# Kernel tuning notes

Measured on AMD Instinct MI355X. Metric: run time of the kernel, lower is better.

## Reference

```python
import jax, jax.numpy as jnp
import numpy as np

N_NODES = 50000
N_EDGES = 600000
N_GRAPHS = 1000


def setup_inputs() -> dict:
    key = jax.random.key(0)
    ks = jax.random.split(key, 16)
    x = jax.random.normal(ks[0], (N_NODES, 37), dtype=jnp.float32)
    edge_index = jax.random.randint(ks[1], (2, N_EDGES), 0, N_NODES, dtype=jnp.int64)
    batch = jnp.sort(jax.random.randint(ks[2], (N_NODES,), 0, N_GRAPHS, dtype=jnp.int64))

    def lin(k, fi, fo):
        s = 1.0 / np.sqrt(fi)
        kw, kb = jax.random.split(k)
        W = jax.random.uniform(kw, (fi, fo), minval=-s, maxval=s, dtype=jnp.float32)
        b = jax.random.uniform(kb, (fo,), minval=-s, maxval=s, dtype=jnp.float32)
        return W, b

    W1, b1 = lin(ks[3], 37, 64)
    W2, b2 = lin(ks[4], 64, 128)
    W3, b3 = lin(ks[5], 128, 64)
    Wf1, bf1 = lin(ks[6], 64, 128)
    Wf2, bf2 = lin(ks[7], 128, 64)
    gamma = jnp.ones((64,), jnp.float32)
    beta = jnp.zeros((64,), jnp.float32)
    return dict(x=x, edge_index=edge_index, batch=batch,
                W1=W1, b1=b1, W2=W2, b2=b2, W3=W3, b3=b3,
                Wf1=Wf1, bf1=bf1, Wf2=Wf2, bf2=bf2, gamma=gamma, beta=beta)


def _gcn_conv(x, W, b, rows, cols, norm, n_nodes):
    # PyG GCNConv: out_i = sum_j norm_ij * (x_j W) + b, over A + I edges
    h = x @ W
    msg = h[rows] * norm[:, None]          # [E+N, F_out] gather
    out = jax.ops.segment_sum(msg, cols, num_segments=n_nodes)  # scatter-add
    return out + b


def reference(x, edge_index, batch,
              W1, b1, W2, b2, W3, b3,
              Wf1, bf1, Wf2, bf2, gamma, beta):
    n = x.shape[0]
    loop = jnp.arange(n, dtype=edge_index.dtype)
    rows = jnp.concatenate([edge_index[0], loop])  # source nodes (+ self loops)
    cols = jnp.concatenate([edge_index[1], loop])  # target nodes
    deg = jax.ops.segment_sum(jnp.ones_like(cols, dtype=x.dtype), cols, num_segments=n)
    dinv = jnp.where(deg > 0, jax.lax.rsqrt(jnp.maximum(deg, 1e-12)), 0.0)
    norm = dinv[rows] * dinv[cols]

    h = jax.nn.relu(_gcn_conv(x, W1, b1, rows, cols, norm, n))
    h = jax.nn.relu(_gcn_conv(h, W2, b2, rows, cols, norm, n))
    h = jax.nn.relu(_gcn_conv(h, W3, b3, rows, cols, norm, n))

    # global mean pool per graph
    sums = jax.ops.segment_sum(h, batch, num_segments=N_GRAPHS)
    cnts = jax.ops.segment_sum(jnp.ones((n,), h.dtype), batch, num_segments=N_GRAPHS)
    g = sums / jnp.maximum(cnts, 1.0)[:, None]

    g = jax.nn.relu(g @ Wf1 + bf1)
    g = jax.nn.relu(g @ Wf2 + bf2)

    mu = jnp.mean(g, axis=-1, keepdims=True)
    var = jnp.mean(jnp.square(g - mu), axis=-1, keepdims=True)
    return (g - mu) * jax.lax.rsqrt(var + 1e-5) * gamma + beta
```

## Files before the change

### kernel.cpp

```cpp
#include <hip/hip_runtime.h>
#include <hip/hip_bf16.h>



__global__ __launch_bounds__(256)
void hist_kernel(const int* __restrict__ cols, int* __restrict__ counts, int E,
                 const int* __restrict__ batch, int* __restrict__ gcnt, int n) {
    int idx = blockIdx.x * 256 + threadIdx.x;
    if (idx < E) {
        atomicAdd(&counts[cols[idx]], 1);
    } else {
        int i = idx - E;
        if (i < n) atomicAdd(&gcnt[batch[i]], 1);
    }
}


__global__ __launch_bounds__(1024)
void scan1_kernel(const int* __restrict__ counts, int* __restrict__ offs,
                  int* __restrict__ bsum, int n) {
    __shared__ int tmp[1024];
    int i = blockIdx.x * 1024 + threadIdx.x;
    int v = (i < n) ? counts[i] : 0;
    tmp[threadIdx.x] = v;
    __syncthreads();
    for (int o = 1; o < 1024; o <<= 1) {
        int x = (threadIdx.x >= o) ? tmp[threadIdx.x - o] : 0;
        __syncthreads();
        tmp[threadIdx.x] += x;
        __syncthreads();
    }
    if (i < n) offs[i] = tmp[threadIdx.x] - v;
    if (threadIdx.x == 1023) bsum[blockIdx.x] = tmp[1023];
}

__global__ __launch_bounds__(1024)
void scan_meta_kernel(int* __restrict__ bsum, int nb,
                      const int* __restrict__ gcnt, int* __restrict__ goff,
                      int ng, int n_nodes) {
    __shared__ int ta[1024];
    __shared__ int tb[1024];
    int t = threadIdx.x;
    int va = (t < nb) ? bsum[t] : 0;
    int vb = (t < ng) ? gcnt[t] : 0;
    ta[t] = va;
    tb[t] = vb;
    __syncthreads();
    for (int o = 1; o < 1024; o <<= 1) {
        int xa = (t >= o) ? ta[t - o] : 0;
        int xb = (t >= o) ? tb[t - o] : 0;
        __syncthreads();
        ta[t] += xa;
        tb[t] += xb;
        __syncthreads();
    }
    if (t < nb) bsum[t] = ta[t] - va;
    if (t < ng) goff[t] = tb[t] - vb;
    if (t == 0) goff[ng] = n_nodes;
}

__global__ __launch_bounds__(256)
void scan3_kernel(int* __restrict__ offs, const int* __restrict__ bsum,
                  const int* __restrict__ counts, float* __restrict__ dinv,
                  int n, int E) {
    int i = blockIdx.x * 256 + threadIdx.x;
    if (i < n) {
        offs[i] += bsum[i >> 10];
        dinv[i] = rsqrtf((float)(counts[i] + 1));
    }
    if (i == 0) offs[n] = E;
}

__global__ __launch_bounds__(256)
void fill_kernel(const int* __restrict__ rows, const int* __restrict__ cols,
                 const int* __restrict__ offs, int* __restrict__ cursor,
                 int* __restrict__ esrc, int E) {
    int e = blockIdx.x * 256 + threadIdx.x;
    if (e >= E) return;
    int r = rows[e], c = cols[e];
    int pos = offs[c] + atomicAdd(&cursor[c], 1);
    esrc[pos] = r;
}


template <int F, int WSRC>
__global__ __launch_bounds__(256)
void agg_kernel(const float* __restrict__ g, const int* __restrict__ offs,
                const int* __restrict__ esrc, const float* __restrict__ dinv,
                const float* __restrict__ bias, int do_relu,
                float* __restrict__ out, int n) {
    static_assert(F <= 64, "one lane per feature");
    int wid  = threadIdx.x >> 6;
    int lane = threadIdx.x & 63;
    int node = blockIdx.x * 4 + wid;
    if (node >= n) return;
    int c = (lane < F) ? lane : (F - 1);
    float dv = dinv[node];
    float a0 = (WSRC ? dv : 1.0f) * g[(size_t)node * F + c];
    float a1 = 0.f, a2 = 0.f, a3 = 0.f, a4 = 0.f, a5 = 0.f, a6 = 0.f, a7 = 0.f;
    int s = offs[node], e = offs[node + 1];
    int k = s;
    for (; k + 7 < e; k += 8) {
        int s0 = esrc[k],     s1 = esrc[k + 1], s2 = esrc[k + 2], s3 = esrc[k + 3];
        int s4 = esrc[k + 4], s5 = esrc[k + 5], s6 = esrc[k + 6], s7 = esrc[k + 7];
        float w0 = WSRC ? dinv[s0] : 1.f, w1 = WSRC ? dinv[s1] : 1.f;
        float w2 = WSRC ? dinv[s2] : 1.f, w3 = WSRC ? dinv[s3] : 1.f;
        float w4 = WSRC ? dinv[s4] : 1.f, w5 = WSRC ? dinv[s5] : 1.f;
        float w6 = WSRC ? dinv[s6] : 1.f, w7 = WSRC ? dinv[s7] : 1.f;
        a0 += w0 * g[(size_t)s0 * F + c];
        a1 += w1 * g[(size_t)s1 * F + c];
        a2 += w2 * g[(size_t)s2 * F + c];
        a3 += w3 * g[(size_t)s3 * F + c];
        a4 += w4 * g[(size_t)s4 * F + c];
        a5 += w5 * g[(size_t)s5 * F + c];
        a6 += w6 * g[(size_t)s6 * F + c];
        a7 += w7 * g[(size_t)s7 * F + c];
    }
    for (; k < e; ++k) {
        int s0 = esrc[k];
        float w0 = WSRC ? dinv[s0] : 1.f;
        a0 += w0 * g[(size_t)s0 * F + c];
    }
    float v = (((a0 + a1) + (a2 + a3)) + ((a4 + a5) + (a6 + a7))) * dv;
    if (bias)    v += bias[c];
    if (do_relu) v = fmaxf(v, 0.f);
    if (lane < F) out[(size_t)node * F + c] = v;
}


template <int K, int F>
__global__ __launch_bounds__(256)
void mm_kernel(const float* __restrict__ X, const float* __restrict__ W,
               const float* __restrict__ bias, const float* __restrict__ dscale,
               int do_relu, float* __restrict__ out, int n) {
    constexpr int ROWS = 32;
    constexpr int CG = F / 4;
    __shared__ __align__(16) float Ws[K * F];
    __shared__ __align__(16) float xs[ROWS * K];
    int r0 = blockIdx.x * ROWS;
    for (int i = threadIdx.x; i < K * F; i += 256) Ws[i] = W[i];
    int nrow = n - r0; if (nrow > ROWS) nrow = ROWS;
    const float* Xb = X + (size_t)r0 * K;
    int tot = nrow * K;
    for (int i = threadIdx.x; i < tot; i += 256) xs[i] = Xb[i];
    __syncthreads();
    for (int idx = threadIdx.x; idx < ROWS * CG; idx += 256) {
        int r = idx / CG, cg = idx % CG;
        if (r >= nrow) break;
        float4 acc = {0.f, 0.f, 0.f, 0.f};
#pragma unroll
        for (int k = 0; k < K; ++k) {
            float xv = xs[r * K + k];
            float4 wv = *reinterpret_cast<const float4*>(&Ws[k * F + cg * 4]);
            acc.x += xv * wv.x; acc.y += xv * wv.y;
            acc.z += xv * wv.z; acc.w += xv * wv.w;
        }
        if (bias) {
            const float4 bv = *reinterpret_cast<const float4*>(&bias[cg * 4]);
            acc.x += bv.x; acc.y += bv.y; acc.z += bv.z; acc.w += bv.w;
        }
        if (do_relu) {
            acc.x = fmaxf(acc.x, 0.f); acc.y = fmaxf(acc.y, 0.f);
            acc.z = fmaxf(acc.z, 0.f); acc.w = fmaxf(acc.w, 0.f);
        }
        if (dscale) {
            float dv = dscale[r0 + r];
            acc.x *= dv; acc.y *= dv; acc.z *= dv; acc.w *= dv;
        }
        *reinterpret_cast<float4*>(&out[(size_t)(r0 + r) * F + cg * 4]) = acc;
    }
}


__global__ __launch_bounds__(256)
void mm23_kernel(const float* __restrict__ X, const float* __restrict__ W2,
                 const float* __restrict__ b2, const float* __restrict__ W3,
                 const float* __restrict__ dinv, float* __restrict__ out, int n) {
    __shared__ __align__(16) float Wbuf[64 * 128];
    __shared__ __align__(16) float Xbuf[32 * 130];
    const int t  = threadIdx.x;
    const int r0 = blockIdx.x * 32;

    for (int i = t * 4; i < 8192; i += 1024)
        *reinterpret_cast<float4*>(&Wbuf[i]) = *reinterpret_cast<const float4*>(&W2[i]);
    for (int idx = t; idx < 32 * 16; idx += 256) {
        int row = idx / 16, col = idx % 16;
        int gr = r0 + row; if (gr >= n) gr = n - 1;
        *reinterpret_cast<float4*>(&Xbuf[row * 68 + col * 4]) =
            *reinterpret_cast<const float4*>(&X[(size_t)gr * 64 + col * 4]);
    }
    __syncthreads();

    const int tc = t % 32, tr = t / 32;
    float4 h2[4];
#pragma unroll
    for (int i = 0; i < 4; ++i) h2[i] = float4{0.f, 0.f, 0.f, 0.f};
#pragma unroll 2
    for (int kk = 0; kk < 64; kk += 4) {
        float4 xv[4];
#pragma unroll
        for (int i = 0; i < 4; ++i)
            xv[i] = *reinterpret_cast<const float4*>(&Xbuf[(tr + 8 * i) * 68 + kk]);
        float4 wv[4];
#pragma unroll
        for (int j = 0; j < 4; ++j)
            wv[j] = *reinterpret_cast<const float4*>(&Wbuf[(kk + j) * 128 + tc * 4]);
#pragma unroll
        for (int i = 0; i < 4; ++i) {
            const float* xp = reinterpret_cast<const float*>(&xv[i]);
#pragma unroll
            for (int j = 0; j < 4; ++j) {
                float s = xp[j];
                h2[i].x += s * wv[j].x; h2[i].y += s * wv[j].y;
                h2[i].z += s * wv[j].z; h2[i].w += s * wv[j].w;
            }
        }
    }
    {
        const float4 bv = *reinterpret_cast<const float4*>(&b2[tc * 4]);
#pragma unroll
        for (int i = 0; i < 4; ++i) {
            h2[i].x = fmaxf(h2[i].x + bv.x, 0.f);
            h2[i].y = fmaxf(h2[i].y + bv.y, 0.f);
            h2[i].z = fmaxf(h2[i].z + bv.z, 0.f);
            h2[i].w = fmaxf(h2[i].w + bv.w, 0.f);
        }
    }
    __syncthreads();

#pragma unroll
    for (int i = 0; i < 4; ++i)
        *reinterpret_cast<float4*>(&Xbuf[(tr + 8 * i) * 130 + tc * 4]) = h2[i];
    for (int i = t * 4; i < 8192; i += 1024)
        *reinterpret_cast<float4*>(&Wbuf[i]) = *reinterpret_cast<const float4*>(&W3[i]);
    __syncthreads();

    const int tc3 = t % 16, tr3 = t / 16;
    float4 q0 = {0.f, 0.f, 0.f, 0.f}, q1 = {0.f, 0.f, 0.f, 0.f};
#pragma unroll 2
    for (int k2 = 0; k2 < 128; k2 += 4) {
        float4 x0 = *reinterpret_cast<const float4*>(&Xbuf[tr3 * 130 + k2]);
        float4 x1 = *reinterpret_cast<const float4*>(&Xbuf[(tr3 + 16) * 130 + k2]);
        float4 wv[4];
#pragma unroll
        for (int j = 0; j < 4; ++j)
            wv[j] = *reinterpret_cast<const float4*>(&Wbuf[(k2 + j) * 64 + tc3 * 4]);
        const float* p0 = reinterpret_cast<const float*>(&x0);
        const float* p1 = reinterpret_cast<const float*>(&x1);
#pragma unroll
        for (int j = 0; j < 4; ++j) {
            float s0 = p0[j], s1 = p1[j];
            q0.x += s0 * wv[j].x; q0.y += s0 * wv[j].y;
            q0.z += s0 * wv[j].z; q0.w += s0 * wv[j].w;
            q1.x += s1 * wv[j].x; q1.y += s1 * wv[j].y;
            q1.z += s1 * wv[j].z; q1.w += s1 * wv[j].w;
        }
    }
    int gr0 = r0 + tr3, gr1 = r0 + tr3 + 16;
    if (gr0 < n) {
        float dv = dinv[gr0];
        q0.x *= dv; q0.y *= dv; q0.z *= dv; q0.w *= dv;
        *reinterpret_cast<float4*>(&out[(size_t)gr0 * 64 + tc3 * 4]) = q0;
    }
    if (gr1 < n) {
        float dv = dinv[gr1];
        q1.x *= dv; q1.y *= dv; q1.z *= dv; q1.w *= dv;
        *reinterpret_cast<float4*>(&out[(size_t)gr1 * 64 + tc3 * 4]) = q1;
    }
}


__global__ __launch_bounds__(128)
void poolmlp_kernel(const float* __restrict__ h, const int* __restrict__ goff,
                    const float* __restrict__ Wf1, const float* __restrict__ bf1,
                    const float* __restrict__ Wf2, const float* __restrict__ bf2,
                    const float* __restrict__ gamma, const float* __restrict__ beta,
                    float* __restrict__ out) {
    __shared__ float red[128];
    __shared__ float gs[64];
    __shared__ float ts[128];
    int g = blockIdx.x, t = threadIdx.x;
    int f = t & 63, half = t >> 6;
    int s = goff[g], e = goff[g + 1];
    float acc = 0.f;
    for (int i = s + half; i < e; i += 2) acc += h[(size_t)i * 64 + f];
    red[t] = acc;
    __syncthreads();
    if (t < 64) {
        float c = (float)(e - s);
        gs[t] = (red[t] + red[t + 64]) / fmaxf(c, 1.0f);
    }
    __syncthreads();
    float a1 = bf1[t];
    for (int k = 0; k < 64; ++k) a1 += gs[k] * Wf1[k * 128 + t];
    ts[t] = fmaxf(a1, 0.f);
    __syncthreads();
    if (t < 64) {
        float a2 = bf2[t];
        for (int k = 0; k < 128; ++k) a2 += ts[k] * Wf2[k * 64 + t];
        float u = fmaxf(a2, 0.f);
        float mu = u;
        for (int o = 1; o < 64; o <<= 1) mu += __shfl_xor(mu, o);
        mu *= (1.0f / 64.0f);
        float d = u - mu;
        float var = d * d;
        for (int o = 1; o < 64; o <<= 1) var += __shfl_xor(var, o);
        var *= (1.0f / 64.0f);
        out[g * 64 + t] = d * rsqrtf(var + 1e-5f) * gamma[t] + beta[t];
    }
}


extern "C" void kernel_launch(void* const* d_in, const int* in_sizes, int n_in,
                              void* d_out, int out_size, void* d_ws, size_t ws_size,
                              hipStream_t stream) {
    const float* x     = (const float*)d_in[0];
    const int*   eidx  = (const int*)d_in[1];
    const int*   batch = (const int*)d_in[2];
    const float* W1 = (const float*)d_in[3];  const float* b1 = (const float*)d_in[4];
    const float* W2 = (const float*)d_in[5];  const float* b2 = (const float*)d_in[6];
    const float* W3 = (const float*)d_in[7];  const float* b3 = (const float*)d_in[8];
    const float* Wf1 = (const float*)d_in[9];  const float* bf1 = (const float*)d_in[10];
    const float* Wf2 = (const float*)d_in[11]; const float* bf2 = (const float*)d_in[12];
    const float* gamma = (const float*)d_in[13]; const float* beta = (const float*)d_in[14];
    float* out = (float*)d_out;

    const int n  = in_sizes[2];
    const int E  = in_sizes[1] / 2;
    const int ng = out_size / 64;
    const int NB = (n + 1023) / 1024;

    const int* rows = eidx;
    const int* cols = eidx + E;

    size_t off = 0;
    auto carve = [&](size_t bytes) {
        void* p = (char*)d_ws + off;
        off += (bytes + 511) & ~(size_t)511;
        return p;
    };
    int*   counts = (int*)  carve((size_t)n * 4);
    int*   cursor = (int*)  carve((size_t)n * 4);
    int*   gcnt   = (int*)  carve((size_t)(ng + 1) * 4);
    size_t zbytes = off;
    int*   offs   = (int*)  carve((size_t)(n + 1) * 4);
    int*   bsum   = (int*)  carve((size_t)(NB + 1) * 4);
    float* dinv   = (float*)carve((size_t)n * 4);
    int*   esrc   = (int*)  carve((size_t)E * 4);
    int*   goff   = (int*)  carve((size_t)(ng + 1) * 4);
    float* bufA   = (float*)carve((size_t)n * 64 * 4);
    float* bufB   = (float*)carve((size_t)n * 64 * 4);
    (void)ws_size;

    hipMemsetAsync(d_ws, 0, zbytes, stream);

    int gH = (E + n + 255) / 256;
    hist_kernel<<<gH, 256, 0, stream>>>(cols, counts, E, batch, gcnt, n);
    scan1_kernel<<<NB, 1024, 0, stream>>>(counts, offs, bsum, n);
    scan_meta_kernel<<<1, 1024, 0, stream>>>(bsum, NB, gcnt, goff, ng, n);
    scan3_kernel<<<(n + 255) / 256, 256, 0, stream>>>(offs, bsum, counts, dinv, n, E);
    fill_kernel<<<(E + 255) / 256, 256, 0, stream>>>(rows, cols, offs, cursor, esrc, E);

    int gagg = (n + 3) / 4;
    agg_kernel<37, 1><<<gagg, 256, 0, stream>>>(x, offs, esrc, dinv, nullptr, 0, bufB, n);
    mm_kernel<37, 64><<<(n + 31) / 32, 256, 0, stream>>>(bufB, W1, b1, dinv, 1, bufA, n);
    agg_kernel<64, 0><<<gagg, 256, 0, stream>>>(bufA, offs, esrc, dinv, nullptr, 0, bufB, n);
    mm23_kernel<<<(n + 31) / 32, 256, 0, stream>>>(bufB, W2, b2, W3, dinv, bufA, n);
    agg_kernel<64, 0><<<gagg, 256, 0, stream>>>(bufA, offs, esrc, dinv, b3, 1, bufB, n);

    poolmlp_kernel<<<ng, 128, 0, stream>>>(bufB, goff, Wf1, bf1, Wf2, bf2, gamma, beta, out);
}
```

Baseline: 332.4 us.

## Fuse CSR build into cooperative kernel and fuse aggregation with dense layers

Replaces the memset plus five CSR-construction kernels with a single cooperative kernel that separates its phases with grid syncs. It also fuses the layer-1 aggregation with the W1 matmul, and the layer-2 aggregation with the W2/W3 matmuls, so the aggregated features stay in LDS instead of going through global memory. This cuts launch count and one global read and write of the intermediate per fused pair. In exchange, the aggregation in the fused kernels is less parallel (each wave handles 8 nodes serially per block), and the cooperative kernel is capped at 1024 blocks with grid-wide sync costs.

New measurement: 893.8 us. 2.69x slower.

```diff
diff --git a/kernel.cpp b/kernel.cpp
--- a/kernel.cpp
+++ b/kernel.cpp
@@ -1,85 +1,291 @@
 #include <hip/hip_runtime.h>
 #include <hip/hip_bf16.h>
+#include <hip/hip_cooperative_groups.h>
+
+namespace cg = cooperative_groups;
 
 
 
 __global__ __launch_bounds__(256)
-void hist_kernel(const int* __restrict__ cols, int* __restrict__ counts, int E,
-                 const int* __restrict__ batch, int* __restrict__ gcnt, int n) {
-    int idx = blockIdx.x * 256 + threadIdx.x;
-    if (idx < E) {
-        atomicAdd(&counts[cols[idx]], 1);
-    } else {
-        int i = idx - E;
-        if (i < n) atomicAdd(&gcnt[batch[i]], 1);
-    }
-}
-
-
-__global__ __launch_bounds__(1024)
-void scan1_kernel(const int* __restrict__ counts, int* __restrict__ offs,
-                  int* __restrict__ bsum, int n) {
-    __shared__ int tmp[1024];
-    int i = blockIdx.x * 1024 + threadIdx.x;
-    int v = (i < n) ? counts[i] : 0;
-    tmp[threadIdx.x] = v;
-    __syncthreads();
-    for (int o = 1; o < 1024; o <<= 1) {
-        int x = (threadIdx.x >= o) ? tmp[threadIdx.x - o] : 0;
+void csr_build_kernel(const int* __restrict__ rows, const int* __restrict__ cols,
+                      const int* __restrict__ batch,
+                      int* counts, int* cursor, int* gcnt,
+                      int* offs, int* bsum, int* goff, float* dinv,
+                      int* esrc, int n, int E, int ng, int NB) {
+    cg::grid_group grid = cg::this_grid();
+    __shared__ int lds[256];
+    const int t   = threadIdx.x;
+    const int gsz = gridDim.x * 256;
+    const int gid = blockIdx.x * 256 + t;
+
+    for (int i = gid; i < n; i += gsz) { counts[i] = 0; cursor[i] = 0; }
+    for (int i = gid; i <= ng; i += gsz) gcnt[i] = 0;
+    grid.sync();
+
+    for (int e = gid; e < E; e += gsz) atomicAdd(&counts[cols[e]], 1);
+    for (int i = gid; i < n; i += gsz) atomicAdd(&gcnt[batch[i]], 1);
+    grid.sync();
+
+    for (int chunk = blockIdx.x; chunk < NB; chunk += gridDim.x) {
+        int i0 = chunk * 1024 + t * 4;
+        int x0 = (i0     < n) ? counts[i0]     : 0;
+        int x1 = (i0 + 1 < n) ? counts[i0 + 1] : 0;
+        int x2 = (i0 + 2 < n) ? counts[i0 + 2] : 0;
+        int x3 = (i0 + 3 < n) ? counts[i0 + 3] : 0;
+        int s0 = x0, s1 = s0 + x1, s2 = s1 + x2, s3 = s2 + x3;
+        lds[t] = s3;
         __syncthreads();
-        tmp[threadIdx.x] += x;
+        for (int o = 1; o < 256; o <<= 1) {
+            int y = (t >= o) ? lds[t - o] : 0;
+            __syncthreads();
+            lds[t] += y;
+            __syncthreads();
+        }
+        int excl = lds[t] - s3;
+        if (i0     < n) offs[i0]     = excl;
+        if (i0 + 1 < n) offs[i0 + 1] = excl + s0;
+        if (i0 + 2 < n) offs[i0 + 2] = excl + s1;
+        if (i0 + 3 < n) offs[i0 + 3] = excl + s2;
+        if (t == 255) bsum[chunk] = excl + s3;
         __syncthreads();
     }
-    if (i < n) offs[i] = tmp[threadIdx.x] - v;
-    if (threadIdx.x == 1023) bsum[blockIdx.x] = tmp[1023];
-}
-
-__global__ __launch_bounds__(1024)
-void scan_meta_kernel(int* __restrict__ bsum, int nb,
-                      const int* __restrict__ gcnt, int* __restrict__ goff,
-                      int ng, int n_nodes) {
-    __shared__ int ta[1024];
-    __shared__ int tb[1024];
-    int t = threadIdx.x;
-    int va = (t < nb) ? bsum[t] : 0;
-    int vb = (t < ng) ? gcnt[t] : 0;
-    ta[t] = va;
-    tb[t] = vb;
-    __syncthreads();
-    for (int o = 1; o < 1024; o <<= 1) {
-        int xa = (t >= o) ? ta[t - o] : 0;
-        int xb = (t >= o) ? tb[t - o] : 0;
+    grid.sync();
+
+    if (blockIdx.x == 0) {
+        int v = (t < NB) ? bsum[t] : 0;
+        lds[t] = v;
         __syncthreads();
-        ta[t] += xa;
-        tb[t] += xb;
+        for (int o = 1; o < 256; o <<= 1) {
+            int y = (t >= o) ? lds[t - o] : 0;
+            __syncthreads();
+            lds[t] += y;
+            __syncthreads();
+        }
+        if (t < NB) bsum[t] = lds[t] - v;
         __syncthreads();
-    }
-    if (t < nb) bsum[t] = ta[t] - va;
-    if (t < ng) goff[t] = tb[t] - vb;
-    if (t == 0) goff[ng] = n_nodes;
-}
-
-__global__ __launch_bounds__(256)
-void scan3_kernel(int* __restrict__ offs, const int* __restrict__ bsum,
-                  const int* __restrict__ counts, float* __restrict__ dinv,
-                  int n, int E) {
-    int i = blockIdx.x * 256 + threadIdx.x;
-    if (i < n) {
+        int i0 = t * 4;
+        int g0 = (i0     < ng) ? gcnt[i0]     : 0;
+        int g1 = (i0 + 1 < ng) ? gcnt[i0 + 1] : 0;
+        int g2 = (i0 + 2 < ng) ? gcnt[i0 + 2] : 0;
+        int g3 = (i0 + 3 < ng) ? gcnt[i0 + 3] : 0;
+        int q0 = g0, q1 = q0 + g1, q2 = q1 + g2, q3 = q2 + g3;
+        lds[t] = q3;
+        __syncthreads();
+        for (int o = 1; o < 256; o <<= 1) {
+            int y = (t >= o) ? lds[t - o] : 0;
+            __syncthreads();
+            lds[t] += y;
+            __syncthreads();
+        }
+        int excl = lds[t] - q3;
+        if (i0     < ng) goff[i0]     = excl;
+        if (i0 + 1 < ng) goff[i0 + 1] = excl + q0;
+        if (i0 + 2 < ng) goff[i0 + 2] = excl + q1;
+        if (i0 + 3 < ng) goff[i0 + 3] = excl + q2;
+        if (t == 0) goff[ng] = n;
+    }
+    grid.sync();
+
+    for (int i = gid; i < n; i += gsz) {
         offs[i] += bsum[i >> 10];
         dinv[i] = rsqrtf((float)(counts[i] + 1));
     }
-    if (i == 0) offs[n] = E;
-}
+    if (gid == 0) offs[n] = E;
+    grid.sync();
+
+    for (int e = gid; e < E; e += gsz) {
+        int r = rows[e], c = cols[e];
+        int pos = offs[c] + atomicAdd(&cursor[c], 1);
+        esrc[pos] = r;
+    }
+}
+
 
 __global__ __launch_bounds__(256)
-void fill_kernel(const int* __restrict__ rows, const int* __restrict__ cols,
-                 const int* __restrict__ offs, int* __restrict__ cursor,
-                 int* __restrict__ esrc, int E) {
-    int e = blockIdx.x * 256 + threadIdx.x;
-    if (e >= E) return;
-    int r = rows[e], c = cols[e];
-    int pos = offs[c] + atomicAdd(&cursor[c], 1);
-    esrc[pos] = r;
+void gcn1_kernel(const float* __restrict__ x, const int* __restrict__ offs,
+                 const int* __restrict__ esrc, const float* __restrict__ dinv,
+                 const float* __restrict__ W1, const float* __restrict__ b1,
+                 float* __restrict__ out, int n) {
+    constexpr int K = 37, F = 64;
+    __shared__ __align__(16) float Ws[K * F];
+    __shared__ float xs[32 * K];
+    const int t = threadIdx.x;
+    const int wid = t >> 6, lane = t & 63;
+    const int r0 = blockIdx.x * 32;
+
+    for (int i = t; i < K * F; i += 256) Ws[i] = W1[i];
+
+    int c = (lane < K) ? lane : (K - 1);
+    for (int p = 0; p < 8; ++p) {
+        int row = wid * 8 + p;
+        int node = r0 + row;
+        if (node >= n) break;
+        float dv = dinv[node];
+        float a0 = dv * x[(size_t)node * K + c];
+        float a1 = 0.f, a2 = 0.f, a3 = 0.f, a4 = 0.f, a5 = 0.f, a6 = 0.f, a7 = 0.f;
+        int s = offs[node], e = offs[node + 1];
+        int k = s;
+        for (; k + 7 < e; k += 8) {
+            int s0 = esrc[k],     s1 = esrc[k + 1], s2 = esrc[k + 2], s3 = esrc[k + 3];
+            int s4 = esrc[k + 4], s5 = esrc[k + 5], s6 = esrc[k + 6], s7 = esrc[k + 7];
+            a0 += dinv[s0] * x[(size_t)s0 * K + c];
+            a1 += dinv[s1] * x[(size_t)s1 * K + c];
+            a2 += dinv[s2] * x[(size_t)s2 * K + c];
+            a3 += dinv[s3] * x[(size_t)s3 * K + c];
+            a4 += dinv[s4] * x[(size_t)s4 * K + c];
+            a5 += dinv[s5] * x[(size_t)s5 * K + c];
+            a6 += dinv[s6] * x[(size_t)s6 * K + c];
+            a7 += dinv[s7] * x[(size_t)s7 * K + c];
+        }
+        for (; k < e; ++k) {
+            int s0 = esrc[k];
+            a0 += dinv[s0] * x[(size_t)s0 * K + c];
+        }
+        float v = (((a0 + a1) + (a2 + a3)) + ((a4 + a5) + (a6 + a7))) * dv;
+        if (lane < K) xs[row * K + c] = v;
+    }
+    __syncthreads();
+
+    int nrow = n - r0; if (nrow > 32) nrow = 32;
+    for (int idx = t; idx < 32 * 16; idx += 256) {
+        int r = idx / 16, cg4 = idx % 16;
+        if (r >= nrow) break;
+        float4 acc = {0.f, 0.f, 0.f, 0.f};
+#pragma unroll
+        for (int k = 0; k < K; ++k) {
+            float xv = xs[r * K + k];
+            float4 wv = *reinterpret_cast<const float4*>(&Ws[k * F + cg4 * 4]);
+            acc.x += xv * wv.x; acc.y += xv * wv.y;
+            acc.z += xv * wv.z; acc.w += xv * wv.w;
+        }
+        const float4 bv = *reinterpret_cast<const float4*>(&b1[cg4 * 4]);
+        float dv = dinv[r0 + r];
+        acc.x = fmaxf(acc.x + bv.x, 0.f) * dv;
+        acc.y = fmaxf(acc.y + bv.y, 0.f) * dv;
+        acc.z = fmaxf(acc.z + bv.z, 0.f) * dv;
+        acc.w = fmaxf(acc.w + bv.w, 0.f) * dv;
+        *reinterpret_cast<float4*>(&out[(size_t)(r0 + r) * F + cg4 * 4]) = acc;
+    }
+}
+
+
+__global__ __launch_bounds__(256)
+void gcn23_kernel(const float* __restrict__ g, const int* __restrict__ offs,
+                  const int* __restrict__ esrc, const float* __restrict__ dinv,
+                  const float* __restrict__ W2, const float* __restrict__ b2,
+                  const float* __restrict__ W3, float* __restrict__ out, int n) {
+    __shared__ __align__(16) float Wbuf[64 * 128];
+    __shared__ __align__(16) float Xbuf[32 * 130];
+    const int t = threadIdx.x;
+    const int wid = t >> 6, lane = t & 63;
+    const int r0 = blockIdx.x * 32;
+
+    for (int i = t * 4; i < 8192; i += 1024)
+        *reinterpret_cast<float4*>(&Wbuf[i]) = *reinterpret_cast<const float4*>(&W2[i]);
+
+    for (int p = 0; p < 8; ++p) {
+        int row = wid * 8 + p;
+        int node = r0 + row;
+        if (node >= n) break;
+        float dv = dinv[node];
+        float a0 = g[(size_t)node * 64 + lane];
+        float a1 = 0.f, a2 = 0.f, a3 = 0.f, a4 = 0.f, a5 = 0.f, a6 = 0.f, a7 = 0.f;
+        int s = offs[node], e = offs[node + 1];
+        int k = s;
+        for (; k + 7 < e; k += 8) {
+            int s0 = esrc[k],     s1 = esrc[k + 1], s2 = esrc[k + 2], s3 = esrc[k + 3];
+            int s4 = esrc[k + 4], s5 = esrc[k + 5], s6 = esrc[k + 6], s7 = esrc[k + 7];
+            a0 += g[(size_t)s0 * 64 + lane];
+            a1 += g[(size_t)s1 * 64 + lane];
+            a2 += g[(size_t)s2 * 64 + lane];
+            a3 += g[(size_t)s3 * 64 + lane];
+            a4 += g[(size_t)s4 * 64 + lane];
+            a5 += g[(size_t)s5 * 64 + lane];
+            a6 += g[(size_t)s6 * 64 + lane];
+            a7 += g[(size_t)s7 * 64 + lane];
+        }
+        for (; k < e; ++k) a0 += g[(size_t)esrc[k] * 64 + lane];
+        Xbuf[row * 68 + lane] =
+            (((a0 + a1) + (a2 + a3)) + ((a4 + a5) + (a6 + a7))) * dv;
+    }
+    __syncthreads();
+
+    const int tc = t % 32, tr = t / 32;
+    float4 h2[4];
+#pragma unroll
+    for (int i = 0; i < 4; ++i) h2[i] = float4{0.f, 0.f, 0.f, 0.f};
+#pragma unroll 2
+    for (int kk = 0; kk < 64; kk += 4) {
+        float4 xv[4];
+#pragma unroll
+        for (int i = 0; i < 4; ++i)
+            xv[i] = *reinterpret_cast<const float4*>(&Xbuf[(tr + 8 * i) * 68 + kk]);
+        float4 wv[4];
+#pragma unroll
+        for (int j = 0; j < 4; ++j)
+            wv[j] = *reinterpret_cast<const float4*>(&Wbuf[(kk + j) * 128 + tc * 4]);
+#pragma unroll
+        for (int i = 0; i < 4; ++i) {
+            const float* xp = reinterpret_cast<const float*>(&xv[i]);
+#pragma unroll
+            for (int j = 0; j < 4; ++j) {
+                float s = xp[j];
+                h2[i].x += s * wv[j].x; h2[i].y += s * wv[j].y;
+                h2[i].z += s * wv[j].z; h2[i].w += s * wv[j].w;
+            }
+        }
+    }
+    {
+        const float4 bv = *reinterpret_cast<const float4*>(&b2[tc * 4]);
+#pragma unroll
+        for (int i = 0; i < 4; ++i) {
+            h2[i].x = fmaxf(h2[i].x + bv.x, 0.f);
+            h2[i].y = fmaxf(h2[i].y + bv.y, 0.f);
+            h2[i].z = fmaxf(h2[i].z + bv.z, 0.f);
+            h2[i].w = fmaxf(h2[i].w + bv.w, 0.f);
+        }
+    }
+    __syncthreads();
+
+#pragma unroll
+    for (int i = 0; i < 4; ++i)
+        *reinterpret_cast<float4*>(&Xbuf[(tr + 8 * i) * 130 + tc * 4]) = h2[i];
+    for (int i = t * 4; i < 8192; i += 1024)
+        *reinterpret_cast<float4*>(&Wbuf[i]) = *reinterpret_cast<const float4*>(&W3[i]);
+    __syncthreads();
+
+    const int tc3 = t % 16, tr3 = t / 16;
+    float4 q0 = {0.f, 0.f, 0.f, 0.f}, q1 = {0.f, 0.f, 0.f, 0.f};
+#pragma unroll 2
+    for (int k2 = 0; k2 < 128; k2 += 4) {
+        float4 x0 = *reinterpret_cast<const float4*>(&Xbuf[tr3 * 130 + k2]);
+        float4 x1 = *reinterpret_cast<const float4*>(&Xbuf[(tr3 + 16) * 130 + k2]);
+        float4 wv[4];
+#pragma unroll
+        for (int j = 0; j < 4; ++j)
+            wv[j] = *reinterpret_cast<const float4*>(&Wbuf[(k2 + j) * 64 + tc3 * 4]);
+        const float* p0 = reinterpret_cast<const float*>(&x0);
+        const float* p1 = reinterpret_cast<const float*>(&x1);
+#pragma unroll
+        for (int j = 0; j < 4; ++j) {
+            float s0 = p0[j], s1 = p1[j];
+            q0.x += s0 * wv[j].x; q0.y += s0 * wv[j].y;
+            q0.z += s0 * wv[j].z; q0.w += s0 * wv[j].w;
+            q1.x += s1 * wv[j].x; q1.y += s1 * wv[j].y;
+            q1.z += s1 * wv[j].z; q1.w += s1 * wv[j].w;
+        }
+    }
+    int gr0 = r0 + tr3, gr1 = r0 + tr3 + 16;
+    if (gr0 < n) {
+        float dv = dinv[gr0];
+        q0.x *= dv; q0.y *= dv; q0.z *= dv; q0.w *= dv;
+        *reinterpret_cast<float4*>(&out[(size_t)gr0 * 64 + tc3 * 4]) = q0;
+    }
+    if (gr1 < n) {
+        float dv = dinv[gr1];
+        q1.x *= dv; q1.y *= dv; q1.z *= dv; q1.w *= dv;
+        *reinterpret_cast<float4*>(&out[(size_t)gr1 * 64 + tc3 * 4]) = q1;
+    }
 }
 
 
@@ -128,148 +334,6 @@
 }
 
 
-template <int K, int F>
-__global__ __launch_bounds__(256)
-void mm_kernel(const float* __restrict__ X, const float* __restrict__ W,
-               const float* __restrict__ bias, const float* __restrict__ dscale,
-               int do_relu, float* __restrict__ out, int n) {
-    constexpr int ROWS = 32;
-    constexpr int CG = F / 4;
-    __shared__ __align__(16) float Ws[K * F];
-    __shared__ __align__(16) float xs[ROWS * K];
-    int r0 = blockIdx.x * ROWS;
-    for (int i = threadIdx.x; i < K * F; i += 256) Ws[i] = W[i];
-    int nrow = n - r0; if (nrow > ROWS) nrow = ROWS;
-    const float* Xb = X + (size_t)r0 * K;
-    int tot = nrow * K;
-    for (int i = threadIdx.x; i < tot; i += 256) xs[i] = Xb[i];
-    __syncthreads();
-    for (int idx = threadIdx.x; idx < ROWS * CG; idx += 256) {
-        int r = idx / CG, cg = idx % CG;
-        if (r >= nrow) break;
-        float4 acc = {0.f, 0.f, 0.f, 0.f};
-#pragma unroll
-        for (int k = 0; k < K; ++k) {
-            float xv = xs[r * K + k];
-            float4 wv = *reinterpret_cast<const float4*>(&Ws[k * F + cg * 4]);
-            acc.x += xv * wv.x; acc.y += xv * wv.y;
-            acc.z += xv * wv.z; acc.w += xv * wv.w;
-        }
-        if (bias) {
-            const float4 bv = *reinterpret_cast<const float4*>(&bias[cg * 4]);
-            acc.x += bv.x; acc.y += bv.y; acc.z += bv.z; acc.w += bv.w;
-        }
-        if (do_relu) {
-            acc.x = fmaxf(acc.x, 0.f); acc.y = fmaxf(acc.y, 0.f);
-            acc.z = fmaxf(acc.z, 0.f); acc.w = fmaxf(acc.w, 0.f);
-        }
-        if (dscale) {
-            float dv = dscale[r0 + r];
-            acc.x *= dv; acc.y *= dv; acc.z *= dv; acc.w *= dv;
-        }
-        *reinterpret_cast<float4*>(&out[(size_t)(r0 + r) * F + cg * 4]) = acc;
-    }
-}
-
-
-__global__ __launch_bounds__(256)
-void mm23_kernel(const float* __restrict__ X, const float* __restrict__ W2,
-                 const float* __restrict__ b2, const float* __restrict__ W3,
-                 const float* __restrict__ dinv, float* __restrict__ out, int n) {
-    __shared__ __align__(16) float Wbuf[64 * 128];
-    __shared__ __align__(16) float Xbuf[32 * 130];
-    const int t  = threadIdx.x;
-    const int r0 = blockIdx.x * 32;
-
-    for (int i = t * 4; i < 8192; i += 1024)
-        *reinterpret_cast<float4*>(&Wbuf[i]) = *reinterpret_cast<const float4*>(&W2[i]);
-    for (int idx = t; idx < 32 * 16; idx += 256) {
-        int row = idx / 16, col = idx % 16;
-        int gr = r0 + row; if (gr >= n) gr = n - 1;
-        *reinterpret_cast<float4*>(&Xbuf[row * 68 + col * 4]) =
-            *reinterpret_cast<const float4*>(&X[(size_t)gr * 64 + col * 4]);
-    }
-    __syncthreads();
-
-    const int tc = t % 32, tr = t / 32;
-    float4 h2[4];
-#pragma unroll
-    for (int i = 0; i < 4; ++i) h2[i] = float4{0.f, 0.f, 0.f, 0.f};
-#pragma unroll 2
-    for (int kk = 0; kk < 64; kk += 4) {
-        float4 xv[4];
-#pragma unroll
-        for (int i = 0; i < 4; ++i)
-            xv[i] = *reinterpret_cast<const float4*>(&Xbuf[(tr + 8 * i) * 68 + kk]);
-        float4 wv[4];
-#pragma unroll
-        for (int j = 0; j < 4; ++j)
-            wv[j] = *reinterpret_cast<const float4*>(&Wbuf[(kk + j) * 128 + tc * 4]);
-#pragma unroll
-        for (int i = 0; i < 4; ++i) {
-            const float* xp = reinterpret_cast<const float*>(&xv[i]);
-#pragma unroll
-            for (int j = 0; j < 4; ++j) {
-                float s = xp[j];
-                h2[i].x += s * wv[j].x; h2[i].y += s * wv[j].y;
-                h2[i].z += s * wv[j].z; h2[i].w += s * wv[j].w;
-            }
-        }
-    }
-    {
-        const float4 bv = *reinterpret_cast<const float4*>(&b2[tc * 4]);
-#pragma unroll
-        for (int i = 0; i < 4; ++i) {
-            h2[i].x = fmaxf(h2[i].x + bv.x, 0.f);
-            h2[i].y = fmaxf(h2[i].y + bv.y, 0.f);
-            h2[i].z = fmaxf(h2[i].z + bv.z, 0.f);
-            h2[i].w = fmaxf(h2[i].w + bv.w, 0.f);
-        }
-    }
-    __syncthreads();
-
-#pragma unroll
-    for (int i = 0; i < 4; ++i)
-        *reinterpret_cast<float4*>(&Xbuf[(tr + 8 * i) * 130 + tc * 4]) = h2[i];
-    for (int i = t * 4; i < 8192; i += 1024)
-        *reinterpret_cast<float4*>(&Wbuf[i]) = *reinterpret_cast<const float4*>(&W3[i]);
-    __syncthreads();
-
-    const int tc3 = t % 16, tr3 = t / 16;
-    float4 q0 = {0.f, 0.f, 0.f, 0.f}, q1 = {0.f, 0.f, 0.f, 0.f};
-#pragma unroll 2
-    for (int k2 = 0; k2 < 128; k2 += 4) {
-        float4 x0 = *reinterpret_cast<const float4*>(&Xbuf[tr3 * 130 + k2]);
-        float4 x1 = *reinterpret_cast<const float4*>(&Xbuf[(tr3 + 16) * 130 + k2]);
-        float4 wv[4];
-#pragma unroll
-        for (int j = 0; j < 4; ++j)
-            wv[j] = *reinterpret_cast<const float4*>(&Wbuf[(k2 + j) * 64 + tc3 * 4]);
-        const float* p0 = reinterpret_cast<const float*>(&x0);
-        const float* p1 = reinterpret_cast<const float*>(&x1);
-#pragma unroll
-        for (int j = 0; j < 4; ++j) {
-            float s0 = p0[j], s1 = p1[j];
-            q0.x += s0 * wv[j].x; q0.y += s0 * wv[j].y;
-            q0.z += s0 * wv[j].z; q0.w += s0 * wv[j].w;
-            q1.x += s1 * wv[j].x; q1.y += s1 * wv[j].y;
-            q1.z += s1 * wv[j].z; q1.w += s1 * wv[j].w;
-        }
-    }
-    int gr0 = r0 + tr3, gr1 = r0 + tr3 + 16;
-    if (gr0 < n) {
-        float dv = dinv[gr0];
-        q0.x *= dv; q0.y *= dv; q0.z *= dv; q0.w *= dv;
-        *reinterpret_cast<float4*>(&out[(size_t)gr0 * 64 + tc3 * 4]) = q0;
-    }
-    if (gr1 < n) {
-        float dv = dinv[gr1];
-        q1.x *= dv; q1.y *= dv; q1.z *= dv; q1.w *= dv;
-        *reinterpret_cast<float4*>(&out[(size_t)gr1 * 64 + tc3 * 4]) = q1;
-    }
-}
-
-
 __global__ __launch_bounds__(128)
 void poolmlp_kernel(const float* __restrict__ h, const int* __restrict__ goff,
                     const float* __restrict__ Wf1, const float* __restrict__ bf1,
@@ -325,10 +389,10 @@
     const float* gamma = (const float*)d_in[13]; const float* beta = (const float*)d_in[14];
     float* out = (float*)d_out;
 
-    const int n  = in_sizes[2];
-    const int E  = in_sizes[1] / 2;
-    const int ng = out_size / 64;
-    const int NB = (n + 1023) / 1024;
+    int n  = in_sizes[2];
+    int E  = in_sizes[1] / 2;
+    int ng = out_size / 64;
+    int NB = (n + 1023) / 1024;
 
     const int* rows = eidx;
     const int* cols = eidx + E;
@@ -342,31 +406,29 @@
     int*   counts = (int*)  carve((size_t)n * 4);
     int*   cursor = (int*)  carve((size_t)n * 4);
     int*   gcnt   = (int*)  carve((size_t)(ng + 1) * 4);
-    size_t zbytes = off;
     int*   offs   = (int*)  carve((size_t)(n + 1) * 4);
     int*   bsum   = (int*)  carve((size_t)(NB + 1) * 4);
+    int*   goff   = (int*)  carve((size_t)(ng + 1) * 4);
     float* dinv   = (float*)carve((size_t)n * 4);
     int*   esrc   = (int*)  carve((size_t)E * 4);
-    int*   goff   = (int*)  carve((size_t)(ng + 1) * 4);
     float* bufA   = (float*)carve((size_t)n * 64 * 4);
     float* bufB   = (float*)carve((size_t)n * 64 * 4);
     (void)ws_size;
 
-    hipMemsetAsync(d_ws, 0, zbytes, stream);
-
-    int gH = (E + n + 255) / 256;
-    hist_kernel<<<gH, 256, 0, stream>>>(cols, counts, E, batch, gcnt, n);
-    scan1_kernel<<<NB, 1024, 0, stream>>>(counts, offs, bsum, n);
-    scan_meta_kernel<<<1, 1024, 0, stream>>>(bsum, NB, gcnt, goff, ng, n);
-    scan3_kernel<<<(n + 255) / 256, 256, 0, stream>>>(offs, bsum, counts, dinv, n, E);
-    fill_kernel<<<(E + 255) / 256, 256, 0, stream>>>(rows, cols, offs, cursor, esrc, E);
-
-    int gagg = (n + 3) / 4;
-    agg_kernel<37, 1><<<gagg, 256, 0, stream>>>(x, offs, esrc, dinv, nullptr, 0, bufB, n);
-    mm_kernel<37, 64><<<(n + 31) / 32, 256, 0, stream>>>(bufB, W1, b1, dinv, 1, bufA, n);
-    agg_kernel<64, 0><<<gagg, 256, 0, stream>>>(bufA, offs, esrc, dinv, nullptr, 0, bufB, n);
-    mm23_kernel<<<(n + 31) / 32, 256, 0, stream>>>(bufB, W2, b2, W3, dinv, bufA, n);
-    agg_kernel<64, 0><<<gagg, 256, 0, stream>>>(bufA, offs, esrc, dinv, b3, 1, bufB, n);
-
-    poolmlp_kernel<<<ng, 128, 0, stream>>>(bufB, goff, Wf1, bf1, Wf2, bf2, gamma, beta, out);
-}
+    {
+        void* args[] = {(void*)&rows, (void*)&cols, (void*)&batch,
+                        (void*)&counts, (void*)&cursor, (void*)&gcnt,
+                        (void*)&offs, (void*)&bsum, (void*)&goff, (void*)&dinv,
+                        (void*)&esrc, (void*)&n, (void*)&E, (void*)&ng, (void*)&NB};
+        hipLaunchCooperativeKernel(reinterpret_cast<void*>(csr_build_kernel),
+                                   dim3(1024), dim3(256), args, 0, stream);
+    }
+
+    int gtile = (n + 31) / 32;
+    gcn1_kernel<<<gtile, 256, 0, stream>>>(x, offs, esrc, dinv, W1, b1, bufA, n);
+    gcn23_kernel<<<gtile, 256, 0, stream>>>(bufA, offs, esrc, dinv, W2, b2, W3, bufB, n);
+    agg_kernel<64, 0><<<(n + 3) / 4, 256, 0, stream>>>(bufB, offs, esrc, dinv, b3, 1,
+                                                       bufA, n);
+
+    poolmlp_kernel<<<ng, 128, 0, stream>>>(bufA, goff, Wf1, bf1, Wf2, bf2, gamma, beta, out);
+}
```
